# Kernel optimization log

Hardware: AMD Instinct MI355X
Metric: run time of the kernel (lower is better)

## Reference

```python
import jax, jax.numpy as jnp
import numpy as np

B, N, D, H = 256, 64, 128, 64

def _w(key, shape, fan_in):
    return jax.random.normal(key, shape, jnp.float32) * (1.0 / np.sqrt(fan_in))

def setup_inputs() -> dict:
    key = jax.random.key(0)
    ks = jax.random.split(key, 6)
    return {
        "observations": jax.random.normal(ks[0], (B, N, D), jnp.float32),
        "enc_w": _w(ks[1], (D, H), D), "enc_b": jnp.zeros((H,), jnp.float32),
        "gate_w1": _w(ks[2], (2 * H, H), 2 * H), "gate_b1": jnp.zeros((H,), jnp.float32),
        "gate_w2": _w(ks[3], (H, 1), H), "gate_b2": jnp.zeros((1,), jnp.float32),
        "msg_w1": _w(ks[4], (H, H), H), "msg_b1": jnp.zeros((H,), jnp.float32),
        "msg_w2": _w(ks[5], (H, H), H), "msg_b2": jnp.zeros((H,), jnp.float32),
    }

def reference(observations, enc_w, enc_b, gate_w1, gate_b1, gate_w2, gate_b2,
              msg_w1, msg_b1, msg_w2, msg_b2):
    # encoder: (B, N, H)
    enc = jax.nn.relu(observations @ enc_w + enc_b)
    h = enc.shape[-1]
    # gate layer 1 on concat([e_i, e_j]) == e_i @ W_top + e_j @ W_bot; avoids
    # materializing the (B, N, N, 2H) concat tensor.
    w_i, w_j = gate_w1[:h], gate_w1[h:]
    gi = enc @ w_i                       # (B, N, H) contribution of receiver i
    gj = enc @ w_j + gate_b1             # (B, N, H) contribution of sender j
    hid = jax.nn.relu(gi[:, :, None, :] + gj[:, None, :, :])   # (B, N, N, H)
    gates = jax.nn.sigmoid(jnp.squeeze(hid @ gate_w2, -1) + gate_b2[0])  # (B, N, N)
    # message_gen(encoded): identical for every i in the original loop
    msg = jax.nn.relu(enc @ msg_w1 + msg_b1) @ msg_w2 + msg_b2  # (B, N, H)
    # enhanced[b, i] = sum_j gates[b, i, j] * msg[b, j]
    enhanced = jnp.einsum('bij,bjh->bih', gates, msg)           # (B, N, H)
    return enhanced
```

## Files before the change

### kernel.cpp

```cpp
#include <hip/hip_runtime.h>

typedef float  f32x4  __attribute__((ext_vector_type(4)));
typedef short  bf16x8 __attribute__((ext_vector_type(8)));

#define Bb 256

__device__ __forceinline__ uint cvtpk(float lo, float hi) {
    uint r;
    asm("v_cvt_pk_bf16_f32 %0, %1, %2" : "=v"(r) : "v"(lo), "v"(hi));
    return r;
}
__device__ __forceinline__ ushort f2b1(float v) { return (ushort)cvtpk(v, v); }

__device__ __forceinline__ void gl_lds16(const void* g, void* l) {
    __builtin_amdgcn_global_load_lds(
        (const __attribute__((address_space(1))) unsigned int*)g,
        (__attribute__((address_space(3))) unsigned int*)l, 16, 0, 0);
}

union U8 { uint u[4]; bf16x8 v; };

__global__ __launch_bounds__(256) void gcm_prep(
    const float* __restrict__ obs, const float* __restrict__ enc_w,
    const float* __restrict__ gate_w1, const float* __restrict__ msg_w1,
    const float* __restrict__ msg_w2,
    ushort* __restrict__ obs_bf, ushort* __restrict__ wimg)
{
    const int bid = blockIdx.x, t = threadIdx.x;
    if (bid < 1024) {
        const int G  = bid * 256 + t;
        const int e0 = G * 8;
        const int b  = e0 >> 13;
        const int r  = (e0 >> 7) & 63;
        const int d0 = e0 & 127;
        const int ds = d0 ^ ((r & 7) << 3);
        const float* src = obs + (((size_t)b * 64 + r) * 128 + ds);
        float4 f0 = *(const float4*)src;
        float4 f1 = *(const float4*)(src + 4);
        uint4 o;
        o.x = cvtpk(f0.x, f0.y); o.y = cvtpk(f0.z, f0.w);
        o.z = cvtpk(f1.x, f1.y); o.w = cvtpk(f1.z, f1.w);
        *(uint4*)(obs_bf + e0) = o;
    } else {
        const int G  = (bid - 1024) * 256 + t;
        const int e0 = G * 8;
        float v[8];
        if (e0 < 8192) {
            const int n  = e0 >> 7;
            const int k0 = (e0 & 127) ^ ((n & 7) << 3);
            #pragma unroll
            for (int j = 0; j < 8; ++j) v[j] = enc_w[(k0 + j) * 64 + n];
        } else {
            const int e  = e0 - 8192;
            const int n  = e >> 6;
            const int k0 = (e & 63) ^ ((n & 7) << 3);
            const float* base; int col;
            if (n < 64)       { base = gate_w1;           col = n;       }
            else if (n < 128) { base = gate_w1 + 64 * 64; col = n - 64;  }
            else if (n < 192) { base = msg_w1;            col = n - 128; }
            else              { base = msg_w2;            col = n - 192; }
            #pragma unroll
            for (int j = 0; j < 8; ++j) v[j] = base[(k0 + j) * 64 + col];
        }
        uint4 o;
        o.x = cvtpk(v[0], v[1]); o.y = cvtpk(v[2], v[3]);
        o.z = cvtpk(v[4], v[5]); o.w = cvtpk(v[6], v[7]);
        *(uint4*)(wimg + e0) = o;
    }
}

__global__ __launch_bounds__(1024, 1) void gcm_main(
    const ushort* __restrict__ obs_bf, const ushort* __restrict__ wimg,
    const float* __restrict__ enc_b, const float* __restrict__ gate_b1,
    const float* __restrict__ gate_w2, const float* __restrict__ gate_b2,
    const float* __restrict__ msg_b1, const float* __restrict__ msg_b2,
    float* __restrict__ out)
{
    const int bb   = blockIdx.x;
    const int t    = threadIdx.x;
    const int lane = t & 63;
    const int wv   = t >> 6;
    const int lr   = lane & 15;
    const int lg   = lane >> 4;
    const int rt   = wv & 3;
    const int ct   = wv >> 2;

    __shared__ __align__(16) char arena[131072];
    ushort* s_obs    = (ushort*)(arena);
    ushort* s_encwT  = (ushort*)(arena + 16384);
    ushort* s_wT     = (ushort*)(arena + 32768);
    ushort* s_enc    = (ushort*)(arena + 65536);
    ushort* s_msgh   = (ushort*)(arena + 73728);
    float*  s_gi     = (float*) (arena + 81920);
    float*  s_gj     = (float*) (arena + 98304);
    ushort* s_msgT   = (ushort*)(arena + 114688);
    ushort* s_gatesb = (ushort*)(arena + 122880);

    {
        const ushort* ob = obs_bf + (size_t)bb * 8192 + wv * 512 + lane * 8;
        gl_lds16(ob, arena + wv * 1024);
        const ushort* ew = wimg + wv * 512 + lane * 8;
        gl_lds16(ew, arena + 16384 + wv * 1024);
        const ushort* w0 = wimg + 8192 + wv * 512 + lane * 8;
        gl_lds16(w0, arena + 32768 + wv * 1024);
        const ushort* w1 = wimg + 8192 + (wv + 16) * 512 + lane * 8;
        gl_lds16(w1, arena + 32768 + (wv + 16) * 1024);
    }
    __syncthreads();

    {
        f32x4 acc = (f32x4){0.f, 0.f, 0.f, 0.f};
        const int arow = rt * 16 + lr;
        const int n = ct * 16 + lr;
        #pragma unroll
        for (int ks = 0; ks < 4; ++ks) {
            const int k0 = ks * 32 + lg * 8;
            bf16x8 a  = *(const bf16x8*)(s_obs + ((arow * 128 + k0) ^ ((arow & 7) << 3)));
            bf16x8 bf = *(const bf16x8*)(s_encwT + ((n * 128 + k0) ^ ((n & 7) << 3)));
            acc = __builtin_amdgcn_mfma_f32_16x16x32_bf16(a, bf, acc, 0, 0, 0);
        }
        const float be = enc_b[n];
        float v0 = fmaxf(acc[0] + be, 0.f), v1 = fmaxf(acc[1] + be, 0.f);
        float v2 = fmaxf(acc[2] + be, 0.f), v3 = fmaxf(acc[3] + be, 0.f);
        uint pA = cvtpk(v0, v1), pB = cvtpk(v2, v3);
        const int rb = rt * 16 + lg * 4;
        s_enc[((rb + 0) * 64 + n) ^ (((rb + 0) & 7) << 3)] = (ushort)pA;
        s_enc[((rb + 1) * 64 + n) ^ (((rb + 1) & 7) << 3)] = (ushort)(pA >> 16);
        s_enc[((rb + 2) * 64 + n) ^ (((rb + 2) & 7) << 3)] = (ushort)pB;
        s_enc[((rb + 3) * 64 + n) ^ (((rb + 3) & 7) << 3)] = (ushort)(pB >> 16);
    }
    __syncthreads();

    {
        f32x4 acc[3];
        #pragma unroll
        for (int q = 0; q < 3; ++q) acc[q] = (f32x4){0.f, 0.f, 0.f, 0.f};
        const int arow = rt * 16 + lr;
        #pragma unroll
        for (int ks = 0; ks < 2; ++ks) {
            const int k0 = ks * 32 + lg * 8;
            bf16x8 a = *(const bf16x8*)(s_enc + ((arow * 64 + k0) ^ ((arow & 7) << 3)));
            #pragma unroll
            for (int q = 0; q < 3; ++q) {
                const int n = (ct * 3 + q) * 16 + lr;
                bf16x8 bf = *(const bf16x8*)(s_wT + ((n * 64 + k0) ^ ((n & 7) << 3)));
                acc[q] = __builtin_amdgcn_mfma_f32_16x16x32_bf16(a, bf, acc[q], 0, 0, 0);
            }
        }
        const int rb = rt * 16 + lg * 4;
        #pragma unroll
        for (int q = 0; q < 3; ++q) {
            const int nfull = (ct * 3 + q) * 16;
            const int cc = nfull + lr;
            if (nfull < 64) {
                #pragma unroll
                for (int rr = 0; rr < 4; ++rr) {
                    const int row = rb + rr;
                    s_gi[(row * 64 + cc) ^ ((row & 7) << 2)] = acc[q][rr];
                }
            } else if (nfull < 128) {
                const float b1 = gate_b1[cc - 64];
                #pragma unroll
                for (int rr = 0; rr < 4; ++rr) {
                    const int row = rb + rr;
                    s_gj[(row * 64 + (cc - 64)) ^ ((row & 7) << 2)] = acc[q][rr] + b1;
                }
            } else {
                const float bm = msg_b1[cc - 128];
                float v0 = fmaxf(acc[q][0] + bm, 0.f), v1 = fmaxf(acc[q][1] + bm, 0.f);
                float v2 = fmaxf(acc[q][2] + bm, 0.f), v3 = fmaxf(acc[q][3] + bm, 0.f);
                uint pA = cvtpk(v0, v1), pB = cvtpk(v2, v3);
                const int c2 = cc - 128;
                s_msgh[((rb + 0) * 64 + c2) ^ (((rb + 0) & 7) << 3)] = (ushort)pA;
                s_msgh[((rb + 1) * 64 + c2) ^ (((rb + 1) & 7) << 3)] = (ushort)(pA >> 16);
                s_msgh[((rb + 2) * 64 + c2) ^ (((rb + 2) & 7) << 3)] = (ushort)pB;
                s_msgh[((rb + 3) * 64 + c2) ^ (((rb + 3) & 7) << 3)] = (ushort)(pB >> 16);
            }
        }
    }
    __syncthreads();

    {
        f32x4 acc = (f32x4){0.f, 0.f, 0.f, 0.f};
        const int arow = rt * 16 + lr;
        const int nn3 = 192 + ct * 16 + lr;
        #pragma unroll
        for (int ks = 0; ks < 2; ++ks) {
            const int k0 = ks * 32 + lg * 8;
            bf16x8 a  = *(const bf16x8*)(s_msgh + ((arow * 64 + k0) ^ ((arow & 7) << 3)));
            bf16x8 bf = *(const bf16x8*)(s_wT + ((nn3 * 64 + k0) ^ ((nn3 & 7) << 3)));
            acc = __builtin_amdgcn_mfma_f32_16x16x32_bf16(a, bf, acc, 0, 0, 0);
        }
        const int h  = ct * 16 + lr;
        const int jb = rt * 16 + lg * 4;
        const float bm2 = msg_b2[h];
        uint pA = cvtpk(acc[0] + bm2, acc[1] + bm2);
        uint pB = cvtpk(acc[2] + bm2, acc[3] + bm2);
        const int e = (h * 64 + jb) ^ ((h & 7) << 3);
        *(uint*)(s_msgT + e)     = pA;
        *(uint*)(s_msgT + e + 2) = pB;
    }

    {
        const int row0g = wv * 4;
        float ag[4] = {0.f, 0.f, 0.f, 0.f};
        #pragma unroll 4
        for (int h0 = 0; h0 < 64; h0 += 4) {
            float4 gj4 = *(const float4*)&s_gj[(lane * 64 + h0) ^ ((lane & 7) << 2)];
            const float4 w24 = *(const float4*)(gate_w2 + h0);
            #pragma unroll
            for (int r = 0; r < 4; ++r) {
                const int row = row0g + r;
                float4 gi4 = *(const float4*)&s_gi[(row * 64 + h0) ^ ((row & 7) << 2)];
                ag[r] = fmaf(fmaxf(gi4.x + gj4.x, 0.f), w24.x, ag[r]);
                ag[r] = fmaf(fmaxf(gi4.y + gj4.y, 0.f), w24.y, ag[r]);
                ag[r] = fmaf(fmaxf(gi4.z + gj4.z, 0.f), w24.z, ag[r]);
                ag[r] = fmaf(fmaxf(gi4.w + gj4.w, 0.f), w24.w, ag[r]);
            }
        }
        const float b2v = gate_b2[0];
        #pragma unroll
        for (int r = 0; r < 4; ++r) {
            const int row = row0g + r;
            const float g = 1.f / (1.f + __expf(-(ag[r] + b2v)));
            s_gatesb[(row * 64 + lane) ^ ((row & 7) << 3)] = f2b1(g);
        }
    }
    __syncthreads();

    {
        const int rtl = wv >> 2;
        const int ctl = wv & 3;
        f32x4 acc = (f32x4){0.f, 0.f, 0.f, 0.f};
        const int arow = rtl * 16 + lr;
        const int n = ctl * 16 + lr;
        #pragma unroll
        for (int ks = 0; ks < 2; ++ks) {
            const int k0 = ks * 32 + lg * 8;
            bf16x8 a  = *(const bf16x8*)(s_gatesb + ((arow * 64 + k0) ^ ((arow & 7) << 3)));
            bf16x8 bf = *(const bf16x8*)(s_msgT   + ((n * 64 + k0) ^ ((n & 7) << 3)));
            acc = __builtin_amdgcn_mfma_f32_16x16x32_bf16(a, bf, acc, 0, 0, 0);
        }
        const int rb = rtl * 16 + lg * 4;
        #pragma unroll
        for (int rr = 0; rr < 4; ++rr)
            out[((size_t)bb * 64 + rb + rr) * 64 + n] = acc[rr];
    }
}

__global__ __launch_bounds__(1024) void gcm_fb(
    const float* __restrict__ obs, const float* __restrict__ enc_w,
    const float* __restrict__ enc_b, const float* __restrict__ gate_w1,
    const float* __restrict__ gate_b1, const float* __restrict__ gate_w2,
    const float* __restrict__ gate_b2, const float* __restrict__ msg_w1,
    const float* __restrict__ msg_b1, const float* __restrict__ msg_w2,
    const float* __restrict__ msg_b2, float* __restrict__ out)
{
    const int bb   = blockIdx.x;
    const int t    = threadIdx.x;
    const int lane = t & 63;
    const int wv   = t >> 6;
    const int lr   = lane & 15;
    const int lg   = lane >> 4;
    const int rt   = wv & 3;
    const int ct   = wv >> 2;

    __shared__ __align__(16) ushort s_encwT[64 * 128];
    __shared__ __align__(16) ushort s_wT[256 * 64];
    __shared__ __align__(16) ushort s_enc[64 * 64];
    __shared__ __align__(16) ushort s_msgh[64 * 64];
    __shared__ __align__(16) ushort s_gatesb[64 * 64];
    __shared__ __align__(16) ushort s_msgT[64 * 64];
    __shared__ __align__(16) float  s_gi[64 * 64];
    __shared__ __align__(16) float  s_gj[64 * 64];
    __shared__ __align__(16) float  s_w2[64];

    float4 pf[8];
    {
        const float* ob = obs + ((size_t)bb * 64 + rt * 16 + lr) * 128 + lg * 8;
        #pragma unroll
        for (int ks = 0; ks < 4; ++ks) {
            pf[2 * ks]     = *(const float4*)(ob + ks * 32);
            pf[2 * ks + 1] = *(const float4*)(ob + ks * 32 + 4);
        }
    }
    if (t < 64) s_w2[t] = gate_w2[t];
    #pragma unroll
    for (int it = 0; it < 2; ++it) {
        const int g  = t + it * 1024;
        const int k  = g >> 4;
        const int n0 = (g & 15) * 4;
        float4 w4 = *(const float4*)(enc_w + k * 64 + n0);
        uint pA = cvtpk(w4.x, w4.y), pB = cvtpk(w4.z, w4.w);
        s_encwT[((n0 + 0) * 128 + k) ^ (((n0 + 0) & 7) << 3)] = (ushort)pA;
        s_encwT[((n0 + 1) * 128 + k) ^ (((n0 + 1) & 7) << 3)] = (ushort)(pA >> 16);
        s_encwT[((n0 + 2) * 128 + k) ^ (((n0 + 2) & 7) << 3)] = (ushort)pB;
        s_encwT[((n0 + 3) * 128 + k) ^ (((n0 + 3) & 7) << 3)] = (ushort)(pB >> 16);
    }
    bf16x8 afrag[4];
    #pragma unroll
    for (int ks = 0; ks < 4; ++ks) {
        U8 u;
        u.u[0] = cvtpk(pf[2 * ks].x,     pf[2 * ks].y);
        u.u[1] = cvtpk(pf[2 * ks].z,     pf[2 * ks].w);
        u.u[2] = cvtpk(pf[2 * ks + 1].x, pf[2 * ks + 1].y);
        u.u[3] = cvtpk(pf[2 * ks + 1].z, pf[2 * ks + 1].w);
        afrag[ks] = u.v;
    }
    float4 pfw[4];
    {
        const int k  = t >> 4;
        const int n0 = (t & 15) * 4;
        pfw[0] = *(const float4*)(gate_w1 + k * 64 + n0);
        pfw[1] = *(const float4*)(gate_w1 + (64 + k) * 64 + n0);
        pfw[2] = *(const float4*)(msg_w1 + k * 64 + n0);
        pfw[3] = *(const float4*)(msg_w2 + k * 64 + n0);
    }
    __syncthreads();
    {
        f32x4 acc = (f32x4){0.f, 0.f, 0.f, 0.f};
        const int n = ct * 16 + lr;
        #pragma unroll
        for (int ks = 0; ks < 4; ++ks) {
            const int k0 = ks * 32 + lg * 8;
            bf16x8 bf = *(const bf16x8*)(s_encwT + ((n * 128 + k0) ^ ((n & 7) << 3)));
            acc = __builtin_amdgcn_mfma_f32_16x16x32_bf16(afrag[ks], bf, acc, 0, 0, 0);
        }
        #pragma unroll
        for (int it = 0; it < 4; ++it) {
            const int k  = t >> 4;
            const int n0 = it * 64 + (t & 15) * 4;
            uint pA = cvtpk(pfw[it].x, pfw[it].y), pB = cvtpk(pfw[it].z, pfw[it].w);
            s_wT[((n0 + 0) * 64 + k) ^ (((n0 + 0) & 7) << 3)] = (ushort)pA;
            s_wT[((n0 + 1) * 64 + k) ^ (((n0 + 1) & 7) << 3)] = (ushort)(pA >> 16);
            s_wT[((n0 + 2) * 64 + k) ^ (((n0 + 2) & 7) << 3)] = (ushort)pB;
            s_wT[((n0 + 3) * 64 + k) ^ (((n0 + 3) & 7) << 3)] = (ushort)(pB >> 16);
        }
        const float be = enc_b[n];
        float v0 = fmaxf(acc[0] + be, 0.f), v1 = fmaxf(acc[1] + be, 0.f);
        float v2 = fmaxf(acc[2] + be, 0.f), v3 = fmaxf(acc[3] + be, 0.f);
        uint pA = cvtpk(v0, v1), pB = cvtpk(v2, v3);
        const int rb = rt * 16 + lg * 4;
        s_enc[((rb + 0) * 64 + n) ^ (((rb + 0) & 7) << 3)] = (ushort)pA;
        s_enc[((rb + 1) * 64 + n) ^ (((rb + 1) & 7) << 3)] = (ushort)(pA >> 16);
        s_enc[((rb + 2) * 64 + n) ^ (((rb + 2) & 7) << 3)] = (ushort)pB;
        s_enc[((rb + 3) * 64 + n) ^ (((rb + 3) & 7) << 3)] = (ushort)(pB >> 16);
    }
    __syncthreads();
    {
        f32x4 acc[3];
        #pragma unroll
        for (int q = 0; q < 3; ++q) acc[q] = (f32x4){0.f, 0.f, 0.f, 0.f};
        const int arow = rt * 16 + lr;
        #pragma unroll
        for (int ks = 0; ks < 2; ++ks) {
            const int k0 = ks * 32 + lg * 8;
            bf16x8 a = *(const bf16x8*)(s_enc + ((arow * 64 + k0) ^ ((arow & 7) << 3)));
            #pragma unroll
            for (int q = 0; q < 3; ++q) {
                const int n = (ct * 3 + q) * 16 + lr;
                bf16x8 bf = *(const bf16x8*)(s_wT + ((n * 64 + k0) ^ ((n & 7) << 3)));
                acc[q] = __builtin_amdgcn_mfma_f32_16x16x32_bf16(a, bf, acc[q], 0, 0, 0);
            }
        }
        const int rb = rt * 16 + lg * 4;
        #pragma unroll
        for (int q = 0; q < 3; ++q) {
            const int nfull = (ct * 3 + q) * 16;
            const int cc = nfull + lr;
            if (nfull < 64) {
                #pragma unroll
                for (int rr = 0; rr < 4; ++rr) {
                    const int row = rb + rr;
                    s_gi[(row * 64 + cc) ^ ((row & 7) << 2)] = acc[q][rr];
                }
            } else if (nfull < 128) {
                const float b1 = gate_b1[cc - 64];
                #pragma unroll
                for (int rr = 0; rr < 4; ++rr) {
                    const int row = rb + rr;
                    s_gj[(row * 64 + (cc - 64)) ^ ((row & 7) << 2)] = acc[q][rr] + b1;
                }
            } else {
                const float bm = msg_b1[cc - 128];
                float v0 = fmaxf(acc[q][0] + bm, 0.f), v1 = fmaxf(acc[q][1] + bm, 0.f);
                float v2 = fmaxf(acc[q][2] + bm, 0.f), v3 = fmaxf(acc[q][3] + bm, 0.f);
                uint pA = cvtpk(v0, v1), pB = cvtpk(v2, v3);
                const int c2 = cc - 128;
                s_msgh[((rb + 0) * 64 + c2) ^ (((rb + 0) & 7) << 3)] = (ushort)pA;
                s_msgh[((rb + 1) * 64 + c2) ^ (((rb + 1) & 7) << 3)] = (ushort)(pA >> 16);
                s_msgh[((rb + 2) * 64 + c2) ^ (((rb + 2) & 7) << 3)] = (ushort)pB;
                s_msgh[((rb + 3) * 64 + c2) ^ (((rb + 3) & 7) << 3)] = (ushort)(pB >> 16);
            }
        }
    }
    __syncthreads();
    {
        f32x4 acc = (f32x4){0.f, 0.f, 0.f, 0.f};
        const int arow = rt * 16 + lr;
        const int nn3 = 192 + ct * 16 + lr;
        #pragma unroll
        for (int ks = 0; ks < 2; ++ks) {
            const int k0 = ks * 32 + lg * 8;
            bf16x8 a = *(const bf16x8*)(s_msgh + ((arow * 64 + k0) ^ ((arow & 7) << 3)));
            bf16x8 bf = *(const bf16x8*)(s_wT + ((nn3 * 64 + k0) ^ ((nn3 & 7) << 3)));
            acc = __builtin_amdgcn_mfma_f32_16x16x32_bf16(a, bf, acc, 0, 0, 0);
        }
        const int h  = ct * 16 + lr;
        const int jb = rt * 16 + lg * 4;
        const float bm2 = msg_b2[h];
        uint pA = cvtpk(acc[0] + bm2, acc[1] + bm2);
        uint pB = cvtpk(acc[2] + bm2, acc[3] + bm2);
        const int e = (h * 64 + jb) ^ ((h & 7) << 3);
        *(uint*)(s_msgT + e)     = pA;
        *(uint*)(s_msgT + e + 2) = pB;
    }
    {
        const int row0g = wv * 4;
        float ag[4] = {0.f, 0.f, 0.f, 0.f};
        #pragma unroll 4
        for (int h0 = 0; h0 < 64; h0 += 4) {
            float4 gj4 = *(const float4*)&s_gj[(lane * 64 + h0) ^ ((lane & 7) << 2)];
            float4 w24 = *(const float4*)&s_w2[h0];
            #pragma unroll
            for (int r = 0; r < 4; ++r) {
                const int row = row0g + r;
                float4 gi4 = *(const float4*)&s_gi[(row * 64 + h0) ^ ((row & 7) << 2)];
                ag[r] = fmaf(fmaxf(gi4.x + gj4.x, 0.f), w24.x, ag[r]);
                ag[r] = fmaf(fmaxf(gi4.y + gj4.y, 0.f), w24.y, ag[r]);
                ag[r] = fmaf(fmaxf(gi4.z + gj4.z, 0.f), w24.z, ag[r]);
                ag[r] = fmaf(fmaxf(gi4.w + gj4.w, 0.f), w24.w, ag[r]);
            }
        }
        const float b2v = gate_b2[0];
        #pragma unroll
        for (int r = 0; r < 4; ++r) {
            const int row = row0g + r;
            const float g = 1.f / (1.f + __expf(-(ag[r] + b2v)));
            s_gatesb[(row * 64 + lane) ^ ((row & 7) << 3)] = f2b1(g);
        }
    }
    __syncthreads();
    {
        const int rtl = wv >> 2;
        const int ctl = wv & 3;
        f32x4 acc = (f32x4){0.f, 0.f, 0.f, 0.f};
        const int arow = rtl * 16 + lr;
        const int n = ctl * 16 + lr;
        #pragma unroll
        for (int ks = 0; ks < 2; ++ks) {
            const int k0 = ks * 32 + lg * 8;
            bf16x8 a  = *(const bf16x8*)(s_gatesb + ((arow * 64 + k0) ^ ((arow & 7) << 3)));
            bf16x8 bf = *(const bf16x8*)(s_msgT   + ((n * 64 + k0) ^ ((n & 7) << 3)));
            acc = __builtin_amdgcn_mfma_f32_16x16x32_bf16(a, bf, acc, 0, 0, 0);
        }
        const int rb = rtl * 16 + lg * 4;
        #pragma unroll
        for (int rr = 0; rr < 4; ++rr)
            out[((size_t)bb * 64 + rb + rr) * 64 + n] = acc[rr];
    }
}

extern "C" void kernel_launch(void* const* d_in, const int* in_sizes, int n_in,
                              void* d_out, int out_size, void* d_ws, size_t ws_size,
                              hipStream_t stream) {
    const float* obs     = (const float*)d_in[0];
    const float* enc_w   = (const float*)d_in[1];
    const float* enc_b   = (const float*)d_in[2];
    const float* gate_w1 = (const float*)d_in[3];
    const float* gate_b1 = (const float*)d_in[4];
    const float* gate_w2 = (const float*)d_in[5];
    const float* gate_b2 = (const float*)d_in[6];
    const float* msg_w1  = (const float*)d_in[7];
    const float* msg_b1  = (const float*)d_in[8];
    const float* msg_w2  = (const float*)d_in[9];
    const float* msg_b2  = (const float*)d_in[10];
    float* out = (float*)d_out;

    const size_t obs_elems = (size_t)Bb * 64 * 128;
    const size_t w_elems   = 24576;
    const size_t need = (obs_elems + w_elems) * sizeof(ushort);
    if (ws_size >= need) {
        ushort* obs_bf = (ushort*)d_ws;
        ushort* wimg   = obs_bf + obs_elems;
        gcm_prep<<<1036, 256, 0, stream>>>(obs, enc_w, gate_w1, msg_w1, msg_w2,
                                           obs_bf, wimg);
        gcm_main<<<Bb, 1024, 0, stream>>>(obs_bf, wimg, enc_b, gate_b1,
                                          gate_w2, gate_b2, msg_b1, msg_b2, out);
    } else {
        gcm_fb<<<Bb, 1024, 0, stream>>>(obs, enc_w, enc_b, gate_w1, gate_b1,
                                        gate_w2, gate_b2, msg_w1, msg_b1,
                                        msg_w2, msg_b2, out);
    }
}
```

Before: 21.61 us.

## Stage gate receiver term as bf16 in global scratch with uniform scalar loads

The receiver-side gate term gi is now written as bf16 into the batch's obs_bf slice in global memory. That slice is already consumed, so it serves as scratch. The gate loop then reads gi through wave-uniform pointers (readfirstlane), so the values can arrive as scalar loads instead of LDS float4 reads. This frees 16 KB of LDS and removes LDS bandwidth pressure in the pairwise gate loop, which is also fully unrolled. The costs are lower precision for gi, reliance on global writes becoming visible after a workgroup barrier, and overwriting the input buffer obs_bf.

New measurement: 21.56 us. No clear change (-0.2%).

```diff
diff --git a/kernel.cpp b/kernel.cpp
--- a/kernel.cpp
+++ b/kernel.cpp
@@ -11,6 +11,8 @@
     return r;
 }
 __device__ __forceinline__ ushort f2b1(float v) { return (ushort)cvtpk(v, v); }
+__device__ __forceinline__ float bflo(uint u) { return __uint_as_float(u << 16); }
+__device__ __forceinline__ float bfhi(uint u) { return __uint_as_float(u & 0xffff0000u); }
 
 __device__ __forceinline__ void gl_lds16(const void* g, void* l) {
     __builtin_amdgcn_global_load_lds(
@@ -70,7 +72,7 @@
 }
 
 __global__ __launch_bounds__(1024, 1) void gcm_main(
-    const ushort* __restrict__ obs_bf, const ushort* __restrict__ wimg,
+    ushort* __restrict__ obs_bf, const ushort* __restrict__ wimg,
     const float* __restrict__ enc_b, const float* __restrict__ gate_b1,
     const float* __restrict__ gate_w2, const float* __restrict__ gate_b2,
     const float* __restrict__ msg_b1, const float* __restrict__ msg_b2,
@@ -85,16 +87,17 @@
     const int rt   = wv & 3;
     const int ct   = wv >> 2;
 
-    __shared__ __align__(16) char arena[131072];
+    __shared__ __align__(16) char arena[114688];
     ushort* s_obs    = (ushort*)(arena);
     ushort* s_encwT  = (ushort*)(arena + 16384);
     ushort* s_wT     = (ushort*)(arena + 32768);
     ushort* s_enc    = (ushort*)(arena + 65536);
     ushort* s_msgh   = (ushort*)(arena + 73728);
-    float*  s_gi     = (float*) (arena + 81920);
-    float*  s_gj     = (float*) (arena + 98304);
-    ushort* s_msgT   = (ushort*)(arena + 114688);
-    ushort* s_gatesb = (ushort*)(arena + 122880);
+    float*  s_gj     = (float*) (arena + 81920);
+    ushort* s_msgT   = (ushort*)(arena + 98304);
+    ushort* s_gatesb = (ushort*)(arena + 106496);
+
+    ushort* gi_ws = obs_bf + (size_t)bb * 8192;
 
     {
         const ushort* ob = obs_bf + (size_t)bb * 8192 + wv * 512 + lane * 8;
@@ -131,6 +134,237 @@
     }
     __syncthreads();
 
+    {
+        f32x4 acc[3];
+        #pragma unroll
+        for (int q = 0; q < 3; ++q) acc[q] = (f32x4){0.f, 0.f, 0.f, 0.f};
+        const int arow = rt * 16 + lr;
+        #pragma unroll
+        for (int ks = 0; ks < 2; ++ks) {
+            const int k0 = ks * 32 + lg * 8;
+            bf16x8 a = *(const bf16x8*)(s_enc + ((arow * 64 + k0) ^ ((arow & 7) << 3)));
+            #pragma unroll
+            for (int q = 0; q < 3; ++q) {
+                const int n = (ct * 3 + q) * 16 + lr;
+                bf16x8 bf = *(const bf16x8*)(s_wT + ((n * 64 + k0) ^ ((n & 7) << 3)));
+                acc[q] = __builtin_amdgcn_mfma_f32_16x16x32_bf16(a, bf, acc[q], 0, 0, 0);
+            }
+        }
+        const int rb = rt * 16 + lg * 4;
+        #pragma unroll
+        for (int q = 0; q < 3; ++q) {
+            const int nfull = (ct * 3 + q) * 16;
+            const int cc = nfull + lr;
+            if (nfull < 64) {
+                #pragma unroll
+                for (int rr = 0; rr < 4; ++rr)
+                    gi_ws[(rb + rr) * 64 + cc] = f2b1(acc[q][rr]);
+            } else if (nfull < 128) {
+                const float b1 = gate_b1[cc - 64];
+                #pragma unroll
+                for (int rr = 0; rr < 4; ++rr) {
+                    const int row = rb + rr;
+                    s_gj[(row * 64 + (cc - 64)) ^ ((row & 7) << 2)] = acc[q][rr] + b1;
+                }
+            } else {
+                const float bm = msg_b1[cc - 128];
+                float v0 = fmaxf(acc[q][0] + bm, 0.f), v1 = fmaxf(acc[q][1] + bm, 0.f);
+                float v2 = fmaxf(acc[q][2] + bm, 0.f), v3 = fmaxf(acc[q][3] + bm, 0.f);
+                uint pA = cvtpk(v0, v1), pB = cvtpk(v2, v3);
+                const int c2 = cc - 128;
+                s_msgh[((rb + 0) * 64 + c2) ^ (((rb + 0) & 7) << 3)] = (ushort)pA;
+                s_msgh[((rb + 1) * 64 + c2) ^ (((rb + 1) & 7) << 3)] = (ushort)(pA >> 16);
+                s_msgh[((rb + 2) * 64 + c2) ^ (((rb + 2) & 7) << 3)] = (ushort)pB;
+                s_msgh[((rb + 3) * 64 + c2) ^ (((rb + 3) & 7) << 3)] = (ushort)(pB >> 16);
+            }
+        }
+    }
+    __syncthreads();
+
+    {
+        f32x4 acc = (f32x4){0.f, 0.f, 0.f, 0.f};
+        const int arow = rt * 16 + lr;
+        const int nn3 = 192 + ct * 16 + lr;
+        #pragma unroll
+        for (int ks = 0; ks < 2; ++ks) {
+            const int k0 = ks * 32 + lg * 8;
+            bf16x8 a  = *(const bf16x8*)(s_msgh + ((arow * 64 + k0) ^ ((arow & 7) << 3)));
+            bf16x8 bf = *(const bf16x8*)(s_wT + ((nn3 * 64 + k0) ^ ((nn3 & 7) << 3)));
+            acc = __builtin_amdgcn_mfma_f32_16x16x32_bf16(a, bf, acc, 0, 0, 0);
+        }
+        const int h  = ct * 16 + lr;
+        const int jb = rt * 16 + lg * 4;
+        const float bm2 = msg_b2[h];
+        uint pA = cvtpk(acc[0] + bm2, acc[1] + bm2);
+        uint pB = cvtpk(acc[2] + bm2, acc[3] + bm2);
+        const int e = (h * 64 + jb) ^ ((h & 7) << 3);
+        *(uint*)(s_msgT + e)     = pA;
+        *(uint*)(s_msgT + e + 2) = pB;
+    }
+
+    {
+        const int row0g = wv * 4;
+        const uint* gip0 = (const uint*)(gi_ws + __builtin_amdgcn_readfirstlane(row0g + 0) * 64);
+        const uint* gip1 = (const uint*)(gi_ws + __builtin_amdgcn_readfirstlane(row0g + 1) * 64);
+        const uint* gip2 = (const uint*)(gi_ws + __builtin_amdgcn_readfirstlane(row0g + 2) * 64);
+        const uint* gip3 = (const uint*)(gi_ws + __builtin_amdgcn_readfirstlane(row0g + 3) * 64);
+        float ag[4] = {0.f, 0.f, 0.f, 0.f};
+        #pragma unroll
+        for (int h0 = 0; h0 < 64; h0 += 4) {
+            float4 gj4 = *(const float4*)&s_gj[(lane * 64 + h0) ^ ((lane & 7) << 2)];
+            const float4 w24 = *(const float4*)(gate_w2 + h0);
+            const int c = h0 >> 1;
+            uint pa, pb;
+            pa = gip0[c]; pb = gip0[c + 1];
+            ag[0] = fmaf(fmaxf(bflo(pa) + gj4.x, 0.f), w24.x, ag[0]);
+            ag[0] = fmaf(fmaxf(bfhi(pa) + gj4.y, 0.f), w24.y, ag[0]);
+            ag[0] = fmaf(fmaxf(bflo(pb) + gj4.z, 0.f), w24.z, ag[0]);
+            ag[0] = fmaf(fmaxf(bfhi(pb) + gj4.w, 0.f), w24.w, ag[0]);
+            pa = gip1[c]; pb = gip1[c + 1];
+            ag[1] = fmaf(fmaxf(bflo(pa) + gj4.x, 0.f), w24.x, ag[1]);
+            ag[1] = fmaf(fmaxf(bfhi(pa) + gj4.y, 0.f), w24.y, ag[1]);
+            ag[1] = fmaf(fmaxf(bflo(pb) + gj4.z, 0.f), w24.z, ag[1]);
+            ag[1] = fmaf(fmaxf(bfhi(pb) + gj4.w, 0.f), w24.w, ag[1]);
+            pa = gip2[c]; pb = gip2[c + 1];
+            ag[2] = fmaf(fmaxf(bflo(pa) + gj4.x, 0.f), w24.x, ag[2]);
+            ag[2] = fmaf(fmaxf(bfhi(pa) + gj4.y, 0.f), w24.y, ag[2]);
+            ag[2] = fmaf(fmaxf(bflo(pb) + gj4.z, 0.f), w24.z, ag[2]);
+            ag[2] = fmaf(fmaxf(bfhi(pb) + gj4.w, 0.f), w24.w, ag[2]);
+            pa = gip3[c]; pb = gip3[c + 1];
+            ag[3] = fmaf(fmaxf(bflo(pa) + gj4.x, 0.f), w24.x, ag[3]);
+            ag[3] = fmaf(fmaxf(bfhi(pa) + gj4.y, 0.f), w24.y, ag[3]);
+            ag[3] = fmaf(fmaxf(bflo(pb) + gj4.z, 0.f), w24.z, ag[3]);
+            ag[3] = fmaf(fmaxf(bfhi(pb) + gj4.w, 0.f), w24.w, ag[3]);
+        }
+        const float b2v = gate_b2[0];
+        #pragma unroll
+        for (int r = 0; r < 4; ++r) {
+            const int row = row0g + r;
+            const float g = 1.f / (1.f + __expf(-(ag[r] + b2v)));
+            s_gatesb[(row * 64 + lane) ^ ((row & 7) << 3)] = f2b1(g);
+        }
+    }
+    __syncthreads();
+
+    {
+        const int rtl = wv >> 2;
+        const int ctl = wv & 3;
+        f32x4 acc = (f32x4){0.f, 0.f, 0.f, 0.f};
+        const int arow = rtl * 16 + lr;
+        const int n = ctl * 16 + lr;
+        #pragma unroll
+        for (int ks = 0; ks < 2; ++ks) {
+            const int k0 = ks * 32 + lg * 8;
+            bf16x8 a  = *(const bf16x8*)(s_gatesb + ((arow * 64 + k0) ^ ((arow & 7) << 3)));
+            bf16x8 bf = *(const bf16x8*)(s_msgT   + ((n * 64 + k0) ^ ((n & 7) << 3)));
+            acc = __builtin_amdgcn_mfma_f32_16x16x32_bf16(a, bf, acc, 0, 0, 0);
+        }
+        const int rb = rtl * 16 + lg * 4;
+        #pragma unroll
+        for (int rr = 0; rr < 4; ++rr)
+            out[((size_t)bb * 64 + rb + rr) * 64 + n] = acc[rr];
+    }
+}
+
+__global__ __launch_bounds__(1024) void gcm_fb(
+    const float* __restrict__ obs, const float* __restrict__ enc_w,
+    const float* __restrict__ enc_b, const float* __restrict__ gate_w1,
+    const float* __restrict__ gate_b1, const float* __restrict__ gate_w2,
+    const float* __restrict__ gate_b2, const float* __restrict__ msg_w1,
+    const float* __restrict__ msg_b1, const float* __restrict__ msg_w2,
+    const float* __restrict__ msg_b2, float* __restrict__ out)
+{
+    const int bb   = blockIdx.x;
+    const int t    = threadIdx.x;
+    const int lane = t & 63;
+    const int wv   = t >> 6;
+    const int lr   = lane & 15;
+    const int lg   = lane >> 4;
+    const int rt   = wv & 3;
+    const int ct   = wv >> 2;
+
+    __shared__ __align__(16) ushort s_encwT[64 * 128];
+    __shared__ __align__(16) ushort s_wT[256 * 64];
+    __shared__ __align__(16) ushort s_enc[64 * 64];
+    __shared__ __align__(16) ushort s_msgh[64 * 64];
+    __shared__ __align__(16) ushort s_gatesb[64 * 64];
+    __shared__ __align__(16) ushort s_msgT[64 * 64];
+    __shared__ __align__(16) float  s_gi[64 * 64];
+    __shared__ __align__(16) float  s_gj[64 * 64];
+    __shared__ __align__(16) float  s_w2[64];
+
+    float4 pf[8];
+    {
+        const float* ob = obs + ((size_t)bb * 64 + rt * 16 + lr) * 128 + lg * 8;
+        #pragma unroll
+        for (int ks = 0; ks < 4; ++ks) {
+            pf[2 * ks]     = *(const float4*)(ob + ks * 32);
+            pf[2 * ks + 1] = *(const float4*)(ob + ks * 32 + 4);
+        }
+    }
+    if (t < 64) s_w2[t] = gate_w2[t];
+    #pragma unroll
+    for (int it = 0; it < 2; ++it) {
+        const int g  = t + it * 1024;
+        const int k  = g >> 4;
+        const int n0 = (g & 15) * 4;
+        float4 w4 = *(const float4*)(enc_w + k * 64 + n0);
+        uint pA = cvtpk(w4.x, w4.y), pB = cvtpk(w4.z, w4.w);
+        s_encwT[((n0 + 0) * 128 + k) ^ (((n0 + 0) & 7) << 3)] = (ushort)pA;
+        s_encwT[((n0 + 1) * 128 + k) ^ (((n0 + 1) & 7) << 3)] = (ushort)(pA >> 16);
+        s_encwT[((n0 + 2) * 128 + k) ^ (((n0 + 2) & 7) << 3)] = (ushort)pB;
+        s_encwT[((n0 + 3) * 128 + k) ^ (((n0 + 3) & 7) << 3)] = (ushort)(pB >> 16);
+    }
+    bf16x8 afrag[4];
+    #pragma unroll
+    for (int ks = 0; ks < 4; ++ks) {
+        U8 u;
+        u.u[0] = cvtpk(pf[2 * ks].x,     pf[2 * ks].y);
+        u.u[1] = cvtpk(pf[2 * ks].z,     pf[2 * ks].w);
+        u.u[2] = cvtpk(pf[2 * ks + 1].x, pf[2 * ks + 1].y);
+        u.u[3] = cvtpk(pf[2 * ks + 1].z, pf[2 * ks + 1].w);
+        afrag[ks] = u.v;
+    }
+    float4 pfw[4];
+    {
+        const int k  = t >> 4;
+        const int n0 = (t & 15) * 4;
+        pfw[0] = *(const float4*)(gate_w1 + k * 64 + n0);
+        pfw[1] = *(const float4*)(gate_w1 + (64 + k) * 64 + n0);
+        pfw[2] = *(const float4*)(msg_w1 + k * 64 + n0);
+        pfw[3] = *(const float4*)(msg_w2 + k * 64 + n0);
+    }
+    __syncthreads();
+    {
+        f32x4 acc = (f32x4){0.f, 0.f, 0.f, 0.f};
+        const int n = ct * 16 + lr;
+        #pragma unroll
+        for (int ks = 0; ks < 4; ++ks) {
+            const int k0 = ks * 32 + lg * 8;
+            bf16x8 bf = *(const bf16x8*)(s_encwT + ((n * 128 + k0) ^ ((n & 7) << 3)));
+            acc = __builtin_amdgcn_mfma_f32_16x16x32_bf16(afrag[ks], bf, acc, 0, 0, 0);
+        }
+        #pragma unroll
+        for (int it = 0; it < 4; ++it) {
+            const int k  = t >> 4;
+            const int n0 = it * 64 + (t & 15) * 4;
+            uint pA = cvtpk(pfw[it].x, pfw[it].y), pB = cvtpk(pfw[it].z, pfw[it].w);
+            s_wT[((n0 + 0) * 64 + k) ^ (((n0 + 0) & 7) << 3)] = (ushort)pA;
+            s_wT[((n0 + 1) * 64 + k) ^ (((n0 + 1) & 7) << 3)] = (ushort)(pA >> 16);
+            s_wT[((n0 + 2) * 64 + k) ^ (((n0 + 2) & 7) << 3)] = (ushort)pB;
+            s_wT[((n0 + 3) * 64 + k) ^ (((n0 + 3) & 7) << 3)] = (ushort)(pB >> 16);
+        }
+        const float be = enc_b[n];
+        float v0 = fmaxf(acc[0] + be, 0.f), v1 = fmaxf(acc[1] + be, 0.f);
+        float v2 = fmaxf(acc[2] + be, 0.f), v3 = fmaxf(acc[3] + be, 0.f);
+        uint pA = cvtpk(v0, v1), pB = cvtpk(v2, v3);
+        const int rb = rt * 16 + lg * 4;
+        s_enc[((rb + 0) * 64 + n) ^ (((rb + 0) & 7) << 3)] = (ushort)pA;
+        s_enc[((rb + 1) * 64 + n) ^ (((rb + 1) & 7) << 3)] = (ushort)(pA >> 16);
+        s_enc[((rb + 2) * 64 + n) ^ (((rb + 2) & 7) << 3)] = (ushort)pB;
+        s_enc[((rb + 3) * 64 + n) ^ (((rb + 3) & 7) << 3)] = (ushort)(pB >> 16);
+    }
+    __syncthreads();
     {
         f32x4 acc[3];
         #pragma unroll
@@ -179,222 +413,6 @@
         }
     }
     __syncthreads();
-
-    {
-        f32x4 acc = (f32x4){0.f, 0.f, 0.f, 0.f};
-        const int arow = rt * 16 + lr;
-        const int nn3 = 192 + ct * 16 + lr;
-        #pragma unroll
-        for (int ks = 0; ks < 2; ++ks) {
-            const int k0 = ks * 32 + lg * 8;
-            bf16x8 a  = *(const bf16x8*)(s_msgh + ((arow * 64 + k0) ^ ((arow & 7) << 3)));
-            bf16x8 bf = *(const bf16x8*)(s_wT + ((nn3 * 64 + k0) ^ ((nn3 & 7) << 3)));
-            acc = __builtin_amdgcn_mfma_f32_16x16x32_bf16(a, bf, acc, 0, 0, 0);
-        }
-        const int h  = ct * 16 + lr;
-        const int jb = rt * 16 + lg * 4;
-        const float bm2 = msg_b2[h];
-        uint pA = cvtpk(acc[0] + bm2, acc[1] + bm2);
-        uint pB = cvtpk(acc[2] + bm2, acc[3] + bm2);
-        const int e = (h * 64 + jb) ^ ((h & 7) << 3);
-        *(uint*)(s_msgT + e)     = pA;
-        *(uint*)(s_msgT + e + 2) = pB;
-    }
-
-    {
-        const int row0g = wv * 4;
-        float ag[4] = {0.f, 0.f, 0.f, 0.f};
-        #pragma unroll 4
-        for (int h0 = 0; h0 < 64; h0 += 4) {
-            float4 gj4 = *(const float4*)&s_gj[(lane * 64 + h0) ^ ((lane & 7) << 2)];
-            const float4 w24 = *(const float4*)(gate_w2 + h0);
-            #pragma unroll
-            for (int r = 0; r < 4; ++r) {
-                const int row = row0g + r;
-                float4 gi4 = *(const float4*)&s_gi[(row * 64 + h0) ^ ((row & 7) << 2)];
-                ag[r] = fmaf(fmaxf(gi4.x + gj4.x, 0.f), w24.x, ag[r]);
-                ag[r] = fmaf(fmaxf(gi4.y + gj4.y, 0.f), w24.y, ag[r]);
-                ag[r] = fmaf(fmaxf(gi4.z + gj4.z, 0.f), w24.z, ag[r]);
-                ag[r] = fmaf(fmaxf(gi4.w + gj4.w, 0.f), w24.w, ag[r]);
-            }
-        }
-        const float b2v = gate_b2[0];
-        #pragma unroll
-        for (int r = 0; r < 4; ++r) {
-            const int row = row0g + r;
-            const float g = 1.f / (1.f + __expf(-(ag[r] + b2v)));
-            s_gatesb[(row * 64 + lane) ^ ((row & 7) << 3)] = f2b1(g);
-        }
-    }
-    __syncthreads();
-
-    {
-        const int rtl = wv >> 2;
-        const int ctl = wv & 3;
-        f32x4 acc = (f32x4){0.f, 0.f, 0.f, 0.f};
-        const int arow = rtl * 16 + lr;
-        const int n = ctl * 16 + lr;
-        #pragma unroll
-        for (int ks = 0; ks < 2; ++ks) {
-            const int k0 = ks * 32 + lg * 8;
-            bf16x8 a  = *(const bf16x8*)(s_gatesb + ((arow * 64 + k0) ^ ((arow & 7) << 3)));
-            bf16x8 bf = *(const bf16x8*)(s_msgT   + ((n * 64 + k0) ^ ((n & 7) << 3)));
-            acc = __builtin_amdgcn_mfma_f32_16x16x32_bf16(a, bf, acc, 0, 0, 0);
-        }
-        const int rb = rtl * 16 + lg * 4;
-        #pragma unroll
-        for (int rr = 0; rr < 4; ++rr)
-            out[((size_t)bb * 64 + rb + rr) * 64 + n] = acc[rr];
-    }
-}
-
-__global__ __launch_bounds__(1024) void gcm_fb(
-    const float* __restrict__ obs, const float* __restrict__ enc_w,
-    const float* __restrict__ enc_b, const float* __restrict__ gate_w1,
-    const float* __restrict__ gate_b1, const float* __restrict__ gate_w2,
-    const float* __restrict__ gate_b2, const float* __restrict__ msg_w1,
-    const float* __restrict__ msg_b1, const float* __restrict__ msg_w2,
-    const float* __restrict__ msg_b2, float* __restrict__ out)
-{
-    const int bb   = blockIdx.x;
-    const int t    = threadIdx.x;
-    const int lane = t & 63;
-    const int wv   = t >> 6;
-    const int lr   = lane & 15;
-    const int lg   = lane >> 4;
-    const int rt   = wv & 3;
-    const int ct   = wv >> 2;
-
-    __shared__ __align__(16) ushort s_encwT[64 * 128];
-    __shared__ __align__(16) ushort s_wT[256 * 64];
-    __shared__ __align__(16) ushort s_enc[64 * 64];
-    __shared__ __align__(16) ushort s_msgh[64 * 64];
-    __shared__ __align__(16) ushort s_gatesb[64 * 64];
-    __shared__ __align__(16) ushort s_msgT[64 * 64];
-    __shared__ __align__(16) float  s_gi[64 * 64];
-    __shared__ __align__(16) float  s_gj[64 * 64];
-    __shared__ __align__(16) float  s_w2[64];
-
-    float4 pf[8];
-    {
-        const float* ob = obs + ((size_t)bb * 64 + rt * 16 + lr) * 128 + lg * 8;
-        #pragma unroll
-        for (int ks = 0; ks < 4; ++ks) {
-            pf[2 * ks]     = *(const float4*)(ob + ks * 32);
-            pf[2 * ks + 1] = *(const float4*)(ob + ks * 32 + 4);
-        }
-    }
-    if (t < 64) s_w2[t] = gate_w2[t];
-    #pragma unroll
-    for (int it = 0; it < 2; ++it) {
-        const int g  = t + it * 1024;
-        const int k  = g >> 4;
-        const int n0 = (g & 15) * 4;
-        float4 w4 = *(const float4*)(enc_w + k * 64 + n0);
-        uint pA = cvtpk(w4.x, w4.y), pB = cvtpk(w4.z, w4.w);
-        s_encwT[((n0 + 0) * 128 + k) ^ (((n0 + 0) & 7) << 3)] = (ushort)pA;
-        s_encwT[((n0 + 1) * 128 + k) ^ (((n0 + 1) & 7) << 3)] = (ushort)(pA >> 16);
-        s_encwT[((n0 + 2) * 128 + k) ^ (((n0 + 2) & 7) << 3)] = (ushort)pB;
-        s_encwT[((n0 + 3) * 128 + k) ^ (((n0 + 3) & 7) << 3)] = (ushort)(pB >> 16);
-    }
-    bf16x8 afrag[4];
-    #pragma unroll
-    for (int ks = 0; ks < 4; ++ks) {
-        U8 u;
-        u.u[0] = cvtpk(pf[2 * ks].x,     pf[2 * ks].y);
-        u.u[1] = cvtpk(pf[2 * ks].z,     pf[2 * ks].w);
-        u.u[2] = cvtpk(pf[2 * ks + 1].x, pf[2 * ks + 1].y);
-        u.u[3] = cvtpk(pf[2 * ks + 1].z, pf[2 * ks + 1].w);
-        afrag[ks] = u.v;
-    }
-    float4 pfw[4];
-    {
-        const int k  = t >> 4;
-        const int n0 = (t & 15) * 4;
-        pfw[0] = *(const float4*)(gate_w1 + k * 64 + n0);
-        pfw[1] = *(const float4*)(gate_w1 + (64 + k) * 64 + n0);
-        pfw[2] = *(const float4*)(msg_w1 + k * 64 + n0);
-        pfw[3] = *(const float4*)(msg_w2 + k * 64 + n0);
-    }
-    __syncthreads();
-    {
-        f32x4 acc = (f32x4){0.f, 0.f, 0.f, 0.f};
-        const int n = ct * 16 + lr;
-        #pragma unroll
-        for (int ks = 0; ks < 4; ++ks) {
-            const int k0 = ks * 32 + lg * 8;
-            bf16x8 bf = *(const bf16x8*)(s_encwT + ((n * 128 + k0) ^ ((n & 7) << 3)));
-            acc = __builtin_amdgcn_mfma_f32_16x16x32_bf16(afrag[ks], bf, acc, 0, 0, 0);
-        }
-        #pragma unroll
-        for (int it = 0; it < 4; ++it) {
-            const int k  = t >> 4;
-            const int n0 = it * 64 + (t & 15) * 4;
-            uint pA = cvtpk(pfw[it].x, pfw[it].y), pB = cvtpk(pfw[it].z, pfw[it].w);
-            s_wT[((n0 + 0) * 64 + k) ^ (((n0 + 0) & 7) << 3)] = (ushort)pA;
-            s_wT[((n0 + 1) * 64 + k) ^ (((n0 + 1) & 7) << 3)] = (ushort)(pA >> 16);
-            s_wT[((n0 + 2) * 64 + k) ^ (((n0 + 2) & 7) << 3)] = (ushort)pB;
-            s_wT[((n0 + 3) * 64 + k) ^ (((n0 + 3) & 7) << 3)] = (ushort)(pB >> 16);
-        }
-        const float be = enc_b[n];
-        float v0 = fmaxf(acc[0] + be, 0.f), v1 = fmaxf(acc[1] + be, 0.f);
-        float v2 = fmaxf(acc[2] + be, 0.f), v3 = fmaxf(acc[3] + be, 0.f);
-        uint pA = cvtpk(v0, v1), pB = cvtpk(v2, v3);
-        const int rb = rt * 16 + lg * 4;
-        s_enc[((rb + 0) * 64 + n) ^ (((rb + 0) & 7) << 3)] = (ushort)pA;
-        s_enc[((rb + 1) * 64 + n) ^ (((rb + 1) & 7) << 3)] = (ushort)(pA >> 16);
-        s_enc[((rb + 2) * 64 + n) ^ (((rb + 2) & 7) << 3)] = (ushort)pB;
-        s_enc[((rb + 3) * 64 + n) ^ (((rb + 3) & 7) << 3)] = (ushort)(pB >> 16);
-    }
-    __syncthreads();
-    {
-        f32x4 acc[3];
-        #pragma unroll
-        for (int q = 0; q < 3; ++q) acc[q] = (f32x4){0.f, 0.f, 0.f, 0.f};
-        const int arow = rt * 16 + lr;
-        #pragma unroll
-        for (int ks = 0; ks < 2; ++ks) {
-            const int k0 = ks * 32 + lg * 8;
-            bf16x8 a = *(const bf16x8*)(s_enc + ((arow * 64 + k0) ^ ((arow & 7) << 3)));
-            #pragma unroll
-            for (int q = 0; q < 3; ++q) {
-                const int n = (ct * 3 + q) * 16 + lr;
-                bf16x8 bf = *(const bf16x8*)(s_wT + ((n * 64 + k0) ^ ((n & 7) << 3)));
-                acc[q] = __builtin_amdgcn_mfma_f32_16x16x32_bf16(a, bf, acc[q], 0, 0, 0);
-            }
-        }
-        const int rb = rt * 16 + lg * 4;
-        #pragma unroll
-        for (int q = 0; q < 3; ++q) {
-            const int nfull = (ct * 3 + q) * 16;
-            const int cc = nfull + lr;
-            if (nfull < 64) {
-                #pragma unroll
-                for (int rr = 0; rr < 4; ++rr) {
-                    const int row = rb + rr;
-                    s_gi[(row * 64 + cc) ^ ((row & 7) << 2)] = acc[q][rr];
-                }
-            } else if (nfull < 128) {
-                const float b1 = gate_b1[cc - 64];
-                #pragma unroll
-                for (int rr = 0; rr < 4; ++rr) {
-                    const int row = rb + rr;
-                    s_gj[(row * 64 + (cc - 64)) ^ ((row & 7) << 2)] = acc[q][rr] + b1;
-                }
-            } else {
-                const float bm = msg_b1[cc - 128];
-                float v0 = fmaxf(acc[q][0] + bm, 0.f), v1 = fmaxf(acc[q][1] + bm, 0.f);
-                float v2 = fmaxf(acc[q][2] + bm, 0.f), v3 = fmaxf(acc[q][3] + bm, 0.f);
-                uint pA = cvtpk(v0, v1), pB = cvtpk(v2, v3);
-                const int c2 = cc - 128;
-                s_msgh[((rb + 0) * 64 + c2) ^ (((rb + 0) & 7) << 3)] = (ushort)pA;
-                s_msgh[((rb + 1) * 64 + c2) ^ (((rb + 1) & 7) << 3)] = (ushort)(pA >> 16);
-                s_msgh[((rb + 2) * 64 + c2) ^ (((rb + 2) & 7) << 3)] = (ushort)pB;
-                s_msgh[((rb + 3) * 64 + c2) ^ (((rb + 3) & 7) << 3)] = (ushort)(pB >> 16);
-            }
-        }
-    }
-    __syncthreads();
     {
         f32x4 acc = (f32x4){0.f, 0.f, 0.f, 0.f};
         const int arow = rt * 16 + lr;
```
